# Kernel tuning notes

Hardware: AMD Instinct MI355X
Metric: run time of the kernel (lower is better)

Reference implementation:

```python
import jax, jax.numpy as jnp
import numpy as np

H = 1024   # LSTM hidden (hardcoded in init_states)
A = 128    # attention / speaker dim
M = 80     # mel channels
TXT = 512  # text embedding dim
E = TXT + A
V = 185    # Flowtron symbol vocab
T = 512    # mel frames
TT = 192   # text tokens
SCALE = 0.05


def setup_inputs() -> dict:
    key = jax.random.key(0)
    ks = jax.random.split(key, 24)
    def rn(k, shape, s=SCALE):
        return jax.random.normal(k, shape, jnp.float32) * s
    return {
        "residual": jax.random.normal(ks[0], (1, M, T), jnp.float32),
        "speaker_vecs": jax.random.normal(ks[1], (1, A), jnp.float32),
        "emb": rn(ks[2], (V, TXT), 1.0),
        "Wih_att": rn(ks[3], (2, 4 * H, M)),
        "Whh_att": rn(ks[4], (2, 4 * H, H)),
        "b_att": jnp.zeros((2, 4 * H), jnp.float32),
        "Wq": rn(ks[5], (2, H, A)),
        "Wk": rn(ks[6], (2, E, A)),
        "Wv": rn(ks[7], (2, E, A)),
        "Wih1": rn(ks[8], (2, 4 * H, H + A)),
        "Whh1": rn(ks[9], (2, 4 * H, H)),
        "b1": jnp.zeros((2, 4 * H), jnp.float32),
        "Wih2": rn(ks[10], (2, 4 * H, H)),
        "Whh2": rn(ks[11], (2, 4 * H, H)),
        "b2": jnp.zeros((2, 4 * H), jnp.float32),
        "Wd": rn(ks[12], (2, H, H)),
        "bd": jnp.zeros((2, H), jnp.float32),
        "Wo": rn(ks[13], (2, H, 2 * M), 0.01),
        "bo": jnp.zeros((2, 2 * M), jnp.float32),
        "Wg": rn(ks[14], (2, H + A, 1)),
        "bg": jnp.zeros((2, 1), jnp.float32),
        "text": jax.random.randint(ks[15], (1, TT), 0, V),
    }


def _cell(x, h, c, Wih, Whh, b):
    # standard LSTM cell, gate order i,f,g,o
    z = x @ Wih.T + h @ Whh.T + b
    i, f, g, o = jnp.split(z, 4, axis=-1)
    c = jax.nn.sigmoid(f) * c + jax.nn.sigmoid(i) * jnp.tanh(g)
    h = jax.nn.sigmoid(o) * jnp.tanh(c)
    return h, c


def _run_flow(seq, enc, p, reverse):
    (Wih_att, Whh_att, b_att, Wq, Wk, Wv, Wih1, Whh1, b1,
     Wih2, Whh2, b2, Wd, bd, Wo, bo, Wg, bg) = p
    keys = enc @ Wk   # [TT, A] precomputed outside the scan
    vals = enc @ Wv   # [TT, A]
    inv = jnp.float32(1.0 / np.sqrt(A))
    def step(carry, x_t):
        prev, ha, ca, h1, c1, h2, c2 = carry
        ha, ca = _cell(prev, ha, ca, Wih_att, Whh_att, b_att)
        attn = jax.nn.softmax((ha @ Wq) @ keys.T * inv, axis=-1)  # [1, TT]
        ctx = attn @ vals                                          # [1, A]
        di = jnp.concatenate([ha, ctx], axis=-1)                   # [1, H+A]
        gate = jax.nn.sigmoid(di @ Wg + bg)  # gate computed; early-exit replaced by full-length scan
        h1, c1 = _cell(di, h1, c1, Wih1, Whh1, b1)
        h2, c2 = _cell(h1, h2, c2, Wih2, Whh2, b2)
        hd = jnp.tanh(h2 @ Wd + bd)
        out = hd @ Wo + bo
        b_p, log_s = jnp.split(out, 2, axis=-1)
        y = (x_t - b_p) * jnp.exp(-log_s)   # inverse affine coupling
        return (y, ha, ca, h1, c1, h2, c2), y
    z0 = jnp.zeros((1, M), seq.dtype)
    zh = jnp.zeros((1, H), seq.dtype)
    xs = seq[::-1] if reverse else seq
    _, ys = jax.lax.scan(step, (z0, zh, zh, zh, zh, zh, zh), xs)  # ys: [T, 1, M]
    return ys[::-1] if reverse else ys


def reference(residual, speaker_vecs, emb, Wih_att, Whh_att, b_att, Wq, Wk, Wv,
              Wih1, Whh1, b1, Wih2, Whh2, b2, Wd, bd, Wo, bo, Wg, bg, text):
    # encoder: text embedding concat broadcast speaker vector -> [TT, E]
    enc = jnp.concatenate(
        [emb[text[0]], jnp.broadcast_to(speaker_vecs, (text.shape[1], speaker_vecs.shape[1]))], axis=-1)
    stacked = (Wih_att, Whh_att, b_att, Wq, Wk, Wv, Wih1, Whh1, b1,
               Wih2, Whh2, b2, Wd, bd, Wo, bo, Wg, bg)
    seq = jnp.transpose(residual, (2, 0, 1))   # [T, 1, M]
    seq = _run_flow(seq, enc, tuple(w[1] for w in stacked), reverse=True)   # backward flow
    seq = _run_flow(seq, enc, tuple(w[0] for w in stacked), reverse=False)  # forward flow
    return jnp.transpose(seq, (1, 2, 0))       # [1, M, T]
```

## Files before the change

### kernel.cpp

```cpp
#include <hip/hip_runtime.h>
#include <hip/hip_bf16.h>
#include <stdint.h>

#define AG __HIP_MEMORY_SCOPE_AGENT
typedef unsigned long long ull;

static constexpr size_t OFF_WA  = 0;
static constexpr size_t OFF_W1  = 18874368;
static constexpr size_t OFF_W2  = 54657024;
static constexpr size_t OFF_WD  = 88342528;
static constexpr size_t OFF_WO  = 92536832;
static constexpr size_t OFF_WQ  = 93192192;
static constexpr size_t OFF_VL  = 93978624;
static constexpr size_t OFF_KEY = 94109696;
static constexpr size_t OFF_V32 = 94306304;
static constexpr size_t OFF_WQT = 94502912;
static constexpr size_t OFF_ENC = 95551488;
static constexpr size_t OFF_RB  = 96043008;
static constexpr size_t OFF_SEQ = 96206848;
static constexpr size_t OFF_DYN = 96370688;
static constexpr size_t OFF_HAb = OFF_DYN + 0;
static constexpr size_t OFF_H1b = OFF_DYN + 4096;
static constexpr size_t OFF_H2b = OFF_DYN + 8192;
static constexpr size_t OFF_HDb = OFF_DYN + 12288;
static constexpr size_t OFF_YBb = OFF_DYN + 16384;
static constexpr size_t OFF_SCb = OFF_DYN + 16896;
static constexpr size_t DYN_BYTES = 18432;
static constexpr size_t NEEDED = OFF_DYN + DYN_BYTES;

__device__ __forceinline__ float aldx(const float* p){ return __hip_atomic_load(p, __ATOMIC_RELAXED, AG); }
__device__ __forceinline__ void  astx(float* p, float v){ __hip_atomic_store(p, v, __ATOMIC_RELAXED, AG); }
__device__ __forceinline__ int   PADI(int k){ return k + ((k>>5)<<2); }
__device__ __forceinline__ float tagf(float f, uint32_t tag){
  return __uint_as_float((__float_as_uint(f) & ~3u) | tag);
}

__device__ __forceinline__ float dot8(uint4 w, const float* v){
  float4 a = *(const float4*)v;
  float4 b = *(const float4*)(v+4);
  float s;
  s = __uint_as_float(w.x << 16) * a.x;
  s = fmaf(__uint_as_float(w.x & 0xffff0000u), a.y, s);
  s = fmaf(__uint_as_float(w.y << 16),         a.z, s);
  s = fmaf(__uint_as_float(w.y & 0xffff0000u), a.w, s);
  s = fmaf(__uint_as_float(w.z << 16),         b.x, s);
  s = fmaf(__uint_as_float(w.z & 0xffff0000u), b.y, s);
  s = fmaf(__uint_as_float(w.w << 16),         b.z, s);
  s = fmaf(__uint_as_float(w.w & 0xffff0000u), b.w, s);
  return s;
}
__device__ __forceinline__ float dot4(uint2 w, const float* v){
  float4 a = *(const float4*)v;
  float s;
  s = __uint_as_float(w.x << 16) * a.x;
  s = fmaf(__uint_as_float(w.x & 0xffff0000u), a.y, s);
  s = fmaf(__uint_as_float(w.y << 16),         a.z, s);
  s = fmaf(__uint_as_float(w.y & 0xffff0000u), a.w, s);
  return s;
}
__device__ __forceinline__ float sigf(float x){ return 1.f/(1.f+__expf(-x)); }
__device__ __forceinline__ float tanhf_(float x){
  x = fminf(12.f, fmaxf(-12.f, x));
  float t = __expf(2.f*x);
  return (t-1.f)/(t+1.f);
}

__global__ void k_init(float* z, int n){ int i = blockIdx.x*256 + threadIdx.x; if (i<n) z[i]=0.f; }

__global__ void k_rbuf(const float* res, float* rb){
  int i = blockIdx.x*256 + threadIdx.x; if (i >= 512*80) return;
  int t = i/80, m = i - t*80;
  rb[i] = res[m*512 + t];
}

__global__ void k_enc(const float* emb, const float* spk, const int* text, float* enc){
  int i = blockIdx.x*256 + threadIdx.x; if (i >= 192*640) return;
  int s = i/640, e = i - s*640;
  enc[i] = (e < 512) ? emb[(size_t)text[s]*512 + e] : spk[e-512];
}

__global__ void k_keysvals(const float* enc, const float* Wk, const float* Wv,
                           float* keys, float* vals32){
  int i = blockIdx.x*256 + threadIdx.x; if (i >= 2*192*128) return;
  int f = i/(192*128); int r = i - f*192*128; int s = r/128, a = r - s*128;
  float ka=0.f, va=0.f;
  for (int e=0;e<640;++e){
    float x = enc[s*640+e];
    ka = fmaf(x, Wk[((size_t)f*640+e)*128+a], ka);
    va = fmaf(x, Wv[((size_t)f*640+e)*128+a], va);
  }
  keys[((size_t)f*192+s)*128+a] = ka;
  vals32[((size_t)f*192+s)*128+a] = va;
}

__global__ void k_wqT(const float* Wq, float* WqT){
  int i = blockIdx.x*256 + threadIdx.x; if (i >= 2*128*1024) return;
  int f = i/(128*1024); int r = i - f*128*1024; int a = r/1024, h = r - a*1024;
  WqT[i] = Wq[((size_t)f*1024+h)*128+a];
}

__global__ void k_wqk2(const float* WqT, const float* keys, uint2* dst){
  int b = blockIdx.x; int f = b/192, s = b - f*192;
  int t = threadIdx.x;
  float4 acc = {0.f,0.f,0.f,0.f};
  const float* kp = keys + ((size_t)f*192+s)*128;
  const float* wp = WqT + (size_t)f*128*1024 + t*4;
  for (int a=0;a<128;++a){
    float kk = kp[a];
    float4 w = *(const float4*)(wp + (size_t)a*1024);
    acc.x = fmaf(kk, w.x, acc.x); acc.y = fmaf(kk, w.y, acc.y);
    acc.z = fmaf(kk, w.z, acc.z); acc.w = fmaf(kk, w.w, acc.w);
  }
  const float inv = 0.08838834764831845f;
  __hip_bfloat16 b0 = __float2bfloat16(acc.x*inv), b1 = __float2bfloat16(acc.y*inv);
  __hip_bfloat16 b2 = __float2bfloat16(acc.z*inv), b3 = __float2bfloat16(acc.w*inv);
  uint2 o;
  o.x = (uint32_t)(*(uint16_t*)&b0) | ((uint32_t)(*(uint16_t*)&b1) << 16);
  o.y = (uint32_t)(*(uint16_t*)&b2) | ((uint32_t)(*(uint16_t*)&b3) << 16);
  dst[((size_t)f*192+s)*256 + t] = o;
}

__device__ __forceinline__ uint32_t pk2(float a, float b){
  __hip_bfloat16 x = __float2bfloat16(a), y = __float2bfloat16(b);
  return (uint32_t)(*(uint16_t*)&x) | ((uint32_t)(*(uint16_t*)&y) << 16);
}

__global__ void k_packV2(const float* vals32, uint4* dst){
  int i = blockIdx.x*256 + threadIdx.x; if (i >= 2*192*16) return;
  int ag = i & 15; int r = i >> 4;
  int s = r % 192; int f = r / 192;
  float v[8];
  for (int e=0;e<8;++e) v[e] = vals32[((size_t)f*192+s)*128 + ag*8 + e];
  uint4 o; o.x = pk2(v[0],v[1]); o.y = pk2(v[2],v[3]); o.z = pk2(v[4],v[5]); o.w = pk2(v[6],v[7]);
  dst[i] = o;
}

__global__ void k_packA2(const float* Wih, const float* Whh, uint4* dst){
  int i = blockIdx.x*256 + threadIdx.x; if (i >= 2*256*256*9) return;
  int j = i % 9; int r = i / 9;
  int t = r & 255; r >>= 8;
  int b = r & 255; int f = r >> 8;
  int rs = t>>4, ks = t&15;
  int row = (rs>>2)*1024 + b*4 + (rs&3);
  float v[8];
  for (int e=0;e<8;++e){
    int c = ks*8 + e;
    if (j == 0) v[e] = (c < 80) ? Wih[((size_t)f*4096+row)*80 + c] : 0.f;
    else        v[e] = Whh[((size_t)f*4096+row)*1024 + (j-1)*128 + c];
  }
  uint4 o; o.x = pk2(v[0],v[1]); o.y = pk2(v[2],v[3]); o.z = pk2(v[4],v[5]); o.w = pk2(v[6],v[7]);
  dst[i] = o;
}

__global__ void k_pack1b(const float* Wih1, const float* Whh1, uint4* dst){
  int i = blockIdx.x*256 + threadIdx.x; if (i >= 2*256*16*273) return;
  int kc = i % 273; int r = i / 273;
  int rr = r & 15; r >>= 4;
  int b = r & 255; int f = r >> 8;
  int row = (rr>>2)*1024 + b*4 + (rr&3);
  int k0 = kc*8;
  float v[8];
  for (int e=0;e<8;++e){
    int k = k0+e; float x;
    if (k < 1024)      x = Wih1[((size_t)f*4096+row)*1152 + k];
    else if (k < 2048) x = Whh1[((size_t)f*4096+row)*1024 + (k-1024)];
    else if (k < 2176) x = Wih1[((size_t)f*4096+row)*1152 + 1024 + (k-2048)];
    else               x = 0.f;
    v[e] = x;
  }
  uint4 o; o.x = pk2(v[0],v[1]); o.y = pk2(v[2],v[3]); o.z = pk2(v[4],v[5]); o.w = pk2(v[6],v[7]);
  dst[i] = o;
}

__global__ void k_pack2b(const float* Wih2, const float* Whh2, uint4* dst){
  int i = blockIdx.x*256 + threadIdx.x; if (i >= 2*256*16*257) return;
  int kc = i % 257; int r = i / 257;
  int rr = r & 15; r >>= 4;
  int b = r & 255; int f = r >> 8;
  int row = (rr>>2)*1024 + b*4 + (rr&3);
  int k0 = kc*8;
  float v[8];
  for (int e=0;e<8;++e){
    int k = k0+e;
    v[e] = (k < 1024) ? Wih2[((size_t)f*4096+row)*1024 + k]
         : (k < 2048) ? Whh2[((size_t)f*4096+row)*1024 + (k-1024)] : 0.f;
  }
  uint4 o; o.x = pk2(v[0],v[1]); o.y = pk2(v[2],v[3]); o.z = pk2(v[4],v[5]); o.w = pk2(v[6],v[7]);
  dst[i] = o;
}

__global__ void k_packD2(const float* Wd, uint4* dst){
  __shared__ float tile[64][65];
  int b = blockIdx.x; int f = b >> 8; int rem = b & 255;
  int ot = rem >> 4, ct = rem & 15;
  int tid = threadIdx.x;
  for (int i = tid; i < 4096; i += 256){
    int rc = i >> 6, oc = i & 63;
    tile[rc][oc] = Wd[((size_t)f*1024 + ct*64 + rc)*1024 + ot*64 + oc];
  }
  __syncthreads();
  for (int w = 0; w < 2; ++w){
    int idx = w*256 + tid;
    int op = idx >> 3, cc = idx & 7;
    int k6 = (ct&7)*8 + cc, j = ct >> 3;
    int o = ot*64 + op;
    int b2 = o >> 2, r2 = o & 3;
    uint4 out;
    out.x = pk2(tile[cc*8+0][op], tile[cc*8+1][op]);
    out.y = pk2(tile[cc*8+2][op], tile[cc*8+3][op]);
    out.z = pk2(tile[cc*8+4][op], tile[cc*8+5][op]);
    out.w = pk2(tile[cc*8+6][op], tile[cc*8+7][op]);
    dst[((((size_t)f*256 + b2)*256) + r2*64 + k6)*2 + j] = out;
  }
}

__global__ void k_packO2(const float* Wo, uint2* dst){
  int i = blockIdx.x*256 + threadIdx.x; if (i >= 2*80*256) return;
  int t = i & 255; int r = i >> 8;
  int m = r % 80; int f = r / 80;
  for (int j = 0; j < 2; ++j){
    int row = m + j*80;
    float v[4];
    for (int e=0;e<4;++e) v[e] = Wo[((size_t)f*1024 + t*4+e)*160 + row];
    uint2 o; o.x = pk2(v[0],v[1]); o.y = pk2(v[2],v[3]);
    dst[(size_t)i*2 + j] = o;
  }
}

__launch_bounds__(256, 1)
__global__ void k_flow6(uint8_t* ws, int fl, int rev, int out_mode,
    const float* b_att_all, const float* b1_all, const float* b2_all,
    const float* bd_all, const float* bo_all,
    const float* xsrc, float* ydst)
{
  const int tid = threadIdx.x, bid = blockIdx.x;
  const int rs = tid >> 4, ks = tid & 15;
  const int wid = tid >> 6;
  const int ko = ks*8 + ((ks>>2)<<2);

  float* habuf = (float*)(ws + OFF_HAb);
  float* h1buf = (float*)(ws + OFF_H1b);
  float* h2buf = (float*)(ws + OFF_H2b);
  float* hdbuf = (float*)(ws + OFF_HDb);
  float* ybuf  = (float*)(ws + OFF_YBb);
  float* scb   = (float*)(ws + OFF_SCb);

  __shared__ __align__(16) ushort W1s[16*2184];
  __shared__ __align__(16) ushort W2s[16*2056];
  __shared__ __align__(16) float haPrevS[1152];
  __shared__ __align__(16) float S2[1152];
  __shared__ __align__(16) float S3[1152];
  __shared__ __align__(16) float scratch[2048];
  __shared__ __align__(16) float yS[144];
  __shared__ __align__(16) float ctxS[144];
  __shared__ __align__(16) float attp[288];
  __shared__ float zred[32];
  __shared__ float cst[3][4];
  __shared__ float bAs[16], b1s[16], b2s[16], bds[4], bos[2];

  const size_t fb = (size_t)fl*256 + bid;

  { const uint4* src = (const uint4*)((const ushort*)(ws + OFF_W1) + fb*16*2184);
    uint4* dst = (uint4*)W1s;
    for (int i = tid; i < 4368; i += 256) dst[i] = src[i]; }
  { const uint4* src = (const uint4*)((const ushort*)(ws + OFF_W2) + fb*16*2056);
    uint4* dst = (uint4*)W2s;
    for (int i = tid; i < 4112; i += 256) dst[i] = src[i]; }
  uint4 wa[9];
  { const uint4* g = (const uint4*)(ws + OFF_WA) + (fb*256 + tid)*9;
    #pragma unroll
    for (int j = 0; j < 9; ++j) wa[j] = g[j]; }
  uint4 wd[2];
  { const uint4* g = (const uint4*)(ws + OFF_WD) + (fb*256 + tid)*2;
    wd[0] = g[0]; wd[1] = g[1]; }
  uint2 wqk = {0,0};
  if (bid < 192) wqk = ((const uint2*)(ws + OFF_WQ))[((size_t)fl*192 + bid)*256 + tid];
  uint4 vals_r[12];
  { const uint4* g = (const uint4*)(ws + OFF_VL) + (((size_t)fl*192 + rs*12)*16 + ks);
    #pragma unroll
    for (int j = 0; j < 12; ++j) vals_r[j] = g[(size_t)j*16]; }
  uint2 wo0 = {0,0}, wo1 = {0,0};
  if (bid < 80){ const uint2* g = (const uint2*)(ws + OFF_WO) + (((size_t)fl*80 + bid)*256 + tid)*2;
    wo0 = g[0]; wo1 = g[1]; }
  if (tid < 16){
    int g = tid >> 2, uu = tid & 3;
    bAs[tid] = b_att_all[fl*4096 + g*1024 + bid*4 + uu];
    b1s[tid] = b1_all  [fl*4096 + g*1024 + bid*4 + uu];
    b2s[tid] = b2_all  [fl*4096 + g*1024 + bid*4 + uu];
  }
  if (tid < 4)  bds[tid] = bd_all[fl*1024 + bid*4 + tid];
  if (tid < 2 && bid < 80) bos[tid] = bo_all[fl*160 + tid*80 + bid];
  if (tid < 12) ((float*)cst)[tid] = 0.f;
  for (int i = tid; i < 1152; i += 256){ haPrevS[i]=0.f; S2[i]=0.f; S3[i]=0.f; }
  if (tid < 144){ yS[tid]=0.f; ctxS[tid]=0.f; }
  __syncthreads();

  auto poll4 = [&](const float* g, float* s, uint32_t tag){
    float v0,v1,v2,v3;
    bool o0=false,o1=false,o2=false,o3=false;
    for(;;){
      if(!o0){ float f=aldx(g+tid);     if((__float_as_uint(f)&3u)==tag){v0=f;o0=true;} }
      if(!o1){ float f=aldx(g+tid+256); if((__float_as_uint(f)&3u)==tag){v1=f;o1=true;} }
      if(!o2){ float f=aldx(g+tid+512); if((__float_as_uint(f)&3u)==tag){v2=f;o2=true;} }
      if(!o3){ float f=aldx(g+tid+768); if((__float_as_uint(f)&3u)==tag){v3=f;o3=true;} }
      if(o0&&o1&&o2&&o3) break;
      __builtin_amdgcn_s_sleep(1);
    }
    s[PADI(tid)]     = v0;  s[PADI(tid+256)] = v1;
    s[PADI(tid+512)] = v2;  s[PADI(tid+768)] = v3;
  };
  auto poll1 = [&](const float* g, int n, float* s, uint32_t tag){
    if (tid < n){
      float f;
      for(;;){ f = aldx(g+tid); if((__float_as_uint(f)&3u)==tag) break;
               __builtin_amdgcn_s_sleep(1); }
      s[PADI(tid)] = f;
    }
  };

  const uint4* w1row = (const uint4*)(W1s) + (size_t)rs*273;
  const uint4* w2row = (const uint4*)(W2s) + (size_t)rs*257;

  float accA = 0.f;

  for (int t = 0; t < 512; ++t) {
    const int col = rev ? (511 - t) : t;
    const uint32_t TAG = (uint32_t)((t+1) & 3);
    float x = 0.f;
    if (bid < 80) x = xsrc[col*80 + bid];

    {
      float acc = accA + dot8(wa[0], yS + ko);
      acc += __shfl_xor(acc,1); acc += __shfl_xor(acc,2);
      acc += __shfl_xor(acc,4); acc += __shfl_xor(acc,8);
      if (ks == 0) zred[rs] = acc + bAs[rs];
    }
    __syncthreads();
    if (tid < 4) {
      float zi=zred[tid], zf=zred[4+tid], zg=zred[8+tid], zo=zred[12+tid];
      float c = sigf(zf)*cst[0][tid] + sigf(zi)*tanhf_(zg);
      float h = sigf(zo)*tanhf_(c);
      cst[0][tid] = c;
      astx(habuf + bid*4 + tid, tagf(h, TAG));
    }

    float acc1 = 0.f, acc2 = 0.f;
    #pragma unroll
    for (int j = 0; j < 8; ++j) acc1 += dot8(w1row[(j+8)*16 + ks], S2 + j*144 + ko);
    #pragma unroll
    for (int j = 0; j < 8; ++j) acc2 += dot8(w2row[(j+8)*16 + ks], S3 + j*144 + ko);

    poll4(habuf, haPrevS, TAG);
    __syncthreads();

    if (bid < 192) {
      float sv = dot4(wqk, haPrevS + tid*4 + ((tid>>3)<<2));
      #pragma unroll
      for (int d=1; d<64; d<<=1) sv += __shfl_xor(sv, d);
      if ((tid&63) == 0) zred[16+wid] = sv;
      __syncthreads();
      if (tid == 0) astx(scb + bid, tagf(zred[16]+zred[17]+zred[18]+zred[19], TAG));
    }

    #pragma unroll
    for (int j = 0; j < 8; ++j) acc1 += dot8(w1row[j*16 + ks], haPrevS + j*144 + ko);

    poll1(scb, 192, attp, TAG);
    __syncthreads();

    {
      float v = (tid < 192) ? attp[PADI(tid)] : -3.0e38f;
      float m = v;
      #pragma unroll
      for (int d=1; d<64; d<<=1) m = fmaxf(m, __shfl_xor(m, d));
      if ((tid&63) == 0) zred[16+wid] = m;
      __syncthreads();
      float mx = fmaxf(fmaxf(zred[16],zred[17]), fmaxf(zred[18],zred[19]));
      float e = (tid < 192) ? __expf(v - mx) : 0.f;
      float sm = e;
      #pragma unroll
      for (int d=1; d<64; d<<=1) sm += __shfl_xor(sm, d);
      if ((tid&63) == 0) zred[20+wid] = sm;
      __syncthreads();
      float inv = 1.f / (zred[20]+zred[21]+zred[22]+zred[23]);
      attp[PADI(tid)] = (tid < 192) ? e * inv : 0.f;
    }
    __syncthreads();
    {
      float pc0=0,pc1=0,pc2=0,pc3=0,pc4=0,pc5=0,pc6=0,pc7=0;
      #pragma unroll
      for (int j = 0; j < 12; ++j){
        float pj = attp[PADI(rs*12 + j)];
        uint4 v = vals_r[j];
        pc0 = fmaf(__uint_as_float(v.x << 16),         pj, pc0);
        pc1 = fmaf(__uint_as_float(v.x & 0xffff0000u), pj, pc1);
        pc2 = fmaf(__uint_as_float(v.y << 16),         pj, pc2);
        pc3 = fmaf(__uint_as_float(v.y & 0xffff0000u), pj, pc3);
        pc4 = fmaf(__uint_as_float(v.z << 16),         pj, pc4);
        pc5 = fmaf(__uint_as_float(v.z & 0xffff0000u), pj, pc5);
        pc6 = fmaf(__uint_as_float(v.w << 16),         pj, pc6);
        pc7 = fmaf(__uint_as_float(v.w & 0xffff0000u), pj, pc7);
      }
      *(float4*)&scratch[tid*8]   = make_float4(pc0,pc1,pc2,pc3);
      *(float4*)&scratch[tid*8+4] = make_float4(pc4,pc5,pc6,pc7);
    }
    __syncthreads();
    if (tid < 128){
      float s = 0.f;
      #pragma unroll
      for (int sg = 0; sg < 16; ++sg) s += scratch[sg*128 + tid];
      ctxS[PADI(tid)] = s;
    }
    __syncthreads();

    {
      acc1 += dot8(w1row[256 + ks], ctxS + ko);
      acc1 += __shfl_xor(acc1,1); acc1 += __shfl_xor(acc1,2);
      acc1 += __shfl_xor(acc1,4); acc1 += __shfl_xor(acc1,8);
      if (ks == 0) zred[rs] = acc1 + b1s[rs];
    }
    __syncthreads();
    if (tid < 4) {
      float zi=zred[tid], zf=zred[4+tid], zg=zred[8+tid], zo=zred[12+tid];
      float c = sigf(zf)*cst[1][tid] + sigf(zi)*tanhf_(zg);
      float h = sigf(zo)*tanhf_(c);
      cst[1][tid] = c;
      astx(h1buf + bid*4 + tid, tagf(h, TAG));
    }

    {
      float a = 0.f;
      #pragma unroll
      for (int j = 1; j < 9; ++j) a += dot8(wa[j], haPrevS + (j-1)*144 + ko);
      accA = a;
    }

    poll4(h1buf, S2, TAG);
    __syncthreads();

    {
      #pragma unroll
      for (int j = 0; j < 8; ++j) acc2 += dot8(w2row[j*16 + ks], S2 + j*144 + ko);
      acc2 += __shfl_xor(acc2,1); acc2 += __shfl_xor(acc2,2);
      acc2 += __shfl_xor(acc2,4); acc2 += __shfl_xor(acc2,8);
      if (ks == 0) zred[rs] = acc2 + b2s[rs];
    }
    __syncthreads();
    if (tid < 4) {
      float zi=zred[tid], zf=zred[4+tid], zg=zred[8+tid], zo=zred[12+tid];
      float c = sigf(zf)*cst[2][tid] + sigf(zi)*tanhf_(zg);
      float h = sigf(zo)*tanhf_(c);
      cst[2][tid] = c;
      astx(h2buf + bid*4 + tid, tagf(h, TAG));
    }

    poll4(h2buf, S3, TAG);
    __syncthreads();

    {
      int k6 = tid & 63, r2 = tid >> 6;
      int kk = k6*8 + ((k6>>2)<<2);
      float acc = dot8(wd[0], S3 + kk) + dot8(wd[1], S3 + 576 + kk);
      #pragma unroll
      for (int d=1; d<64; d<<=1) acc += __shfl_xor(acc, d);
      if (k6 == 0) astx(hdbuf + bid*4 + r2, tagf(tanhf_(acc + bds[r2]), TAG));
    }

    if (bid < 80) {
      poll4(hdbuf, scratch, TAG);
      __syncthreads();
      int po = tid*4 + ((tid>>3)<<2);
      float pb = dot4(wo0, scratch + po);
      float pl = dot4(wo1, scratch + po);
      #pragma unroll
      for (int d=1; d<64; d<<=1) { pb += __shfl_xor(pb, d); pl += __shfl_xor(pl, d); }
      if ((tid & 63) == 0) { zred[16+wid] = pb; zred[20+wid] = pl; }
      __syncthreads();
      if (tid == 0) {
        float bp = zred[16]+zred[17]+zred[18]+zred[19] + bos[0];
        float ls = zred[20]+zred[21]+zred[22]+zred[23] + bos[1];
        float y = (x - bp) * __expf(-ls);
        if (out_mode == 0) ydst[col*80 + bid] = y;
        else               ydst[bid*512 + col] = y;
        astx(ybuf + bid, tagf(y, TAG));
      }
    }

    poll1(ybuf, 80, yS, TAG);
    __syncthreads();
  }
}

extern "C" void kernel_launch(void* const* d_in, const int* in_sizes, int n_in,
                              void* d_out, int out_size, void* d_ws, size_t ws_size,
                              hipStream_t stream) {
  if (ws_size < NEEDED) return;
  uint8_t* ws = (uint8_t*)d_ws;
  const float* residual = (const float*)d_in[0];
  const float* spk      = (const float*)d_in[1];
  const float* emb      = (const float*)d_in[2];
  const float* Wih_att  = (const float*)d_in[3];
  const float* Whh_att  = (const float*)d_in[4];
  const float* b_att    = (const float*)d_in[5];
  const float* Wq       = (const float*)d_in[6];
  const float* Wk       = (const float*)d_in[7];
  const float* Wv       = (const float*)d_in[8];
  const float* Wih1     = (const float*)d_in[9];
  const float* Whh1     = (const float*)d_in[10];
  const float* b1       = (const float*)d_in[11];
  const float* Wih2     = (const float*)d_in[12];
  const float* Whh2     = (const float*)d_in[13];
  const float* b2       = (const float*)d_in[14];
  const float* Wd       = (const float*)d_in[15];
  const float* bd       = (const float*)d_in[16];
  const float* Wo       = (const float*)d_in[17];
  const float* bo       = (const float*)d_in[18];
  const int*   text     = (const int*)d_in[21];

  dim3 B(256);
  k_rbuf<<<160, B, 0, stream>>>(residual, (float*)(ws+OFF_RB));
  k_enc<<<480, B, 0, stream>>>(emb, spk, text, (float*)(ws+OFF_ENC));
  k_keysvals<<<192, B, 0, stream>>>((const float*)(ws+OFF_ENC), Wk, Wv,
                                    (float*)(ws+OFF_KEY), (float*)(ws+OFF_V32));
  k_wqT<<<1024, B, 0, stream>>>(Wq, (float*)(ws+OFF_WQT));
  k_wqk2<<<384, B, 0, stream>>>((const float*)(ws+OFF_WQT), (const float*)(ws+OFF_KEY),
                                (uint2*)(ws+OFF_WQ));
  k_packV2<<<24, B, 0, stream>>>((const float*)(ws+OFF_V32), (uint4*)(ws+OFF_VL));
  k_packA2<<<4608, B, 0, stream>>>(Wih_att, Whh_att, (uint4*)(ws+OFF_WA));
  k_pack1b<<<8736, B, 0, stream>>>(Wih1, Whh1, (uint4*)(ws+OFF_W1));
  k_pack2b<<<8224, B, 0, stream>>>(Wih2, Whh2, (uint4*)(ws+OFF_W2));
  k_packD2<<<512, B, 0, stream>>>(Wd, (uint4*)(ws+OFF_WD));
  k_packO2<<<160, B, 0, stream>>>(Wo, (uint2*)(ws+OFF_WO));

  k_init<<<18, B, 0, stream>>>((float*)(ws+OFF_DYN), (int)(DYN_BYTES/4));
  k_flow6<<<256, B, 0, stream>>>(ws, 1, 1, 0, b_att, b1, b2, bd, bo,
                                 (const float*)(ws+OFF_RB), (float*)(ws+OFF_SEQ));
  k_init<<<18, B, 0, stream>>>((float*)(ws+OFF_DYN), (int)(DYN_BYTES/4));
  k_flow6<<<256, B, 0, stream>>>(ws, 0, 0, 1, b_att, b1, b2, bd, bo,
                                 (const float*)(ws+OFF_SEQ), (float*)d_out);
}
```

Baseline: 24.96 ms.

## Relay cross-block broadcasts through 32 relay blocks into per-group mirror buffers

Replaces direct polling of the single global handoff buffers by all 256 blocks with a two-level broadcast. The first 32 blocks poll the root buffer and copy tagged values into one of 32 mirror regions, and the remaining blocks poll the mirror region matching their low block bits. The aim is to cut contention on the hot cache lines that every block spins on at each step. In exchange, each handoff gains an extra store-then-load hop of latency, and the larger workspace needs a longer init kernel.

New measurement: 32.71 ms. +31.0%, slower.

```diff
diff --git a/kernel.cpp b/kernel.cpp
--- a/kernel.cpp
+++ b/kernel.cpp
@@ -25,7 +25,13 @@
 static constexpr size_t OFF_HDb = OFF_DYN + 12288;
 static constexpr size_t OFF_YBb = OFF_DYN + 16384;
 static constexpr size_t OFF_SCb = OFF_DYN + 16896;
-static constexpr size_t DYN_BYTES = 18432;
+static constexpr size_t OFF_RHA = OFF_DYN + 18432;
+static constexpr size_t OFF_RH1 = OFF_RHA + 131072;
+static constexpr size_t OFF_RH2 = OFF_RH1 + 131072;
+static constexpr size_t OFF_RHD = OFF_RH2 + 131072;
+static constexpr size_t OFF_RSC = OFF_RHD + 131072;
+static constexpr size_t OFF_RYB = OFF_RSC + 32768;
+static constexpr size_t DYN_BYTES = 18432 + 4*131072 + 32768 + 16384;
 static constexpr size_t NEEDED = OFF_DYN + DYN_BYTES;
 
 __device__ __forceinline__ float aldx(const float* p){ return __hip_atomic_load(p, __ATOMIC_RELAXED, AG); }
@@ -228,7 +234,7 @@
 }
 
 __launch_bounds__(256, 1)
-__global__ void k_flow6(uint8_t* ws, int fl, int rev, int out_mode,
+__global__ void k_flow7(uint8_t* ws, int fl, int rev, int out_mode,
     const float* b_att_all, const float* b1_all, const float* b2_all,
     const float* bd_all, const float* bo_all,
     const float* xsrc, float* ydst)
@@ -237,6 +243,8 @@
   const int rs = tid >> 4, ks = tid & 15;
   const int wid = tid >> 6;
   const int ko = ks*8 + ((ks>>2)<<2);
+  const bool isRelay = (bid < 32);
+  const int rsel = bid & 31;
 
   float* habuf = (float*)(ws + OFF_HAb);
   float* h1buf = (float*)(ws + OFF_H1b);
@@ -244,6 +252,12 @@
   float* hdbuf = (float*)(ws + OFF_HDb);
   float* ybuf  = (float*)(ws + OFF_YBb);
   float* scb   = (float*)(ws + OFF_SCb);
+  float* rha = (float*)(ws + OFF_RHA) + rsel*1024;
+  float* rh1 = (float*)(ws + OFF_RH1) + rsel*1024;
+  float* rh2 = (float*)(ws + OFF_RH2) + rsel*1024;
+  float* rhd = (float*)(ws + OFF_RHD) + rsel*1024;
+  float* rsc = (float*)(ws + OFF_RSC) + rsel*256;
+  float* ryb = (float*)(ws + OFF_RYB) + rsel*128;
 
   __shared__ __align__(16) ushort W1s[16*2184];
   __shared__ __align__(16) ushort W2s[16*2056];
@@ -295,8 +309,9 @@
   if (tid < 144){ yS[tid]=0.f; ctxS[tid]=0.f; }
   __syncthreads();
 
-  auto poll4 = [&](const float* g, float* s, uint32_t tag){
+  auto bc4 = [&](const float* root, float* region, float* s, uint32_t tag){
     float v0,v1,v2,v3;
+    const float* g = isRelay ? root : region;
     bool o0=false,o1=false,o2=false,o3=false;
     for(;;){
       if(!o0){ float f=aldx(g+tid);     if((__float_as_uint(f)&3u)==tag){v0=f;o0=true;} }
@@ -306,14 +321,20 @@
       if(o0&&o1&&o2&&o3) break;
       __builtin_amdgcn_s_sleep(1);
     }
+    if (isRelay){
+      astx(region+tid, v0); astx(region+tid+256, v1);
+      astx(region+tid+512, v2); astx(region+tid+768, v3);
+    }
     s[PADI(tid)]     = v0;  s[PADI(tid+256)] = v1;
     s[PADI(tid+512)] = v2;  s[PADI(tid+768)] = v3;
   };
-  auto poll1 = [&](const float* g, int n, float* s, uint32_t tag){
+  auto bc1 = [&](const float* root, float* region, int n, float* s, uint32_t tag){
     if (tid < n){
+      const float* g = isRelay ? root : region;
       float f;
       for(;;){ f = aldx(g+tid); if((__float_as_uint(f)&3u)==tag) break;
                __builtin_amdgcn_s_sleep(1); }
+      if (isRelay) astx(region+tid, f);
       s[PADI(tid)] = f;
     }
   };
@@ -350,7 +371,7 @@
     #pragma unroll
     for (int j = 0; j < 8; ++j) acc2 += dot8(w2row[(j+8)*16 + ks], S3 + j*144 + ko);
 
-    poll4(habuf, haPrevS, TAG);
+    bc4(habuf, rha, haPrevS, TAG);
     __syncthreads();
 
     if (bid < 192) {
@@ -365,7 +386,7 @@
     #pragma unroll
     for (int j = 0; j < 8; ++j) acc1 += dot8(w1row[j*16 + ks], haPrevS + j*144 + ko);
 
-    poll1(scb, 192, attp, TAG);
+    bc1(scb, rsc, 192, attp, TAG);
     __syncthreads();
 
     {
@@ -435,7 +456,7 @@
       accA = a;
     }
 
-    poll4(h1buf, S2, TAG);
+    bc4(h1buf, rh1, S2, TAG);
     __syncthreads();
 
     {
@@ -454,7 +475,7 @@
       astx(h2buf + bid*4 + tid, tagf(h, TAG));
     }
 
-    poll4(h2buf, S3, TAG);
+    bc4(h2buf, rh2, S3, TAG);
     __syncthreads();
 
     {
@@ -467,7 +488,7 @@
     }
 
     if (bid < 80) {
-      poll4(hdbuf, scratch, TAG);
+      bc4(hdbuf, rhd, scratch, TAG);
       __syncthreads();
       int po = tid*4 + ((tid>>3)<<2);
       float pb = dot4(wo0, scratch + po);
@@ -486,7 +507,7 @@
       }
     }
 
-    poll1(ybuf, 80, yS, TAG);
+    bc1(ybuf, ryb, 80, yS, TAG);
     __syncthreads();
   }
 }
@@ -532,10 +553,10 @@
   k_packD2<<<512, B, 0, stream>>>(Wd, (uint4*)(ws+OFF_WD));
   k_packO2<<<160, B, 0, stream>>>(Wo, (uint2*)(ws+OFF_WO));
 
-  k_init<<<18, B, 0, stream>>>((float*)(ws+OFF_DYN), (int)(DYN_BYTES/4));
-  k_flow6<<<256, B, 0, stream>>>(ws, 1, 1, 0, b_att, b1, b2, bd, bo,
+  k_init<<<579, B, 0, stream>>>((float*)(ws+OFF_DYN), (int)(DYN_BYTES/4));
+  k_flow7<<<256, B, 0, stream>>>(ws, 1, 1, 0, b_att, b1, b2, bd, bo,
                                  (const float*)(ws+OFF_RB), (float*)(ws+OFF_SEQ));
-  k_init<<<18, B, 0, stream>>>((float*)(ws+OFF_DYN), (int)(DYN_BYTES/4));
-  k_flow6<<<256, B, 0, stream>>>(ws, 0, 0, 1, b_att, b1, b2, bd, bo,
+  k_init<<<579, B, 0, stream>>>((float*)(ws+OFF_DYN), (int)(DYN_BYTES/4));
+  k_flow7<<<256, B, 0, stream>>>(ws, 0, 0, 1, b_att, b1, b2, bd, bo,
                                  (const float*)(ws+OFF_SEQ), (float*)d_out);
 }
```
